# Kernel optimization log

Hardware: AMD Instinct MI355X
Metric: run time of the kernel (lower is better)

## Reference

```python
import jax, jax.numpy as jnp
import numpy as np

N_NODES = 100000
N_EDGES = 3200000
D_IN = 128
D_OUT = 128


def setup_inputs() -> dict:
    key = jax.random.key(0)
    kx, kw, kb, kr, kc, kv = jax.random.split(key, 6)
    x = jax.random.normal(kx, (N_NODES, D_IN), dtype=jnp.float32)
    W = jax.random.normal(kw, (D_OUT, D_IN), dtype=jnp.float32) * (1.0 / np.sqrt(D_IN))
    b = jax.random.normal(kb, (D_OUT,), dtype=jnp.float32) * 0.01
    adj_rows = jax.random.randint(kr, (N_EDGES,), 0, N_NODES, dtype=jnp.int32)
    adj_cols = jax.random.randint(kc, (N_EDGES,), 0, N_NODES, dtype=jnp.int32)
    adj_vals = jax.random.uniform(kv, (N_EDGES,), dtype=jnp.float32)
    return {"x": x, "W": W, "b": b, "adj_rows": adj_rows,
            "adj_cols": adj_cols, "adj_vals": adj_vals}


def reference(x, W, b, adj_rows, adj_cols, adj_vals):
    # linear: out = x @ W.T + b   -> [N, D_OUT]
    out = jnp.einsum('ni,oi->no', x, W) + b
    # spmm(adj, out): row r = sum over edges (r, c, v) of v * out[c]
    gathered = out[adj_cols] * adj_vals[:, None]          # [E, D_OUT]
    agg = jax.ops.segment_sum(gathered, adj_rows, num_segments=x.shape[0])
    return jax.nn.elu(agg)
```

## Files before the change

### kernel.cpp

```cpp
#include <hip/hip_runtime.h>
#include <hip/hip_bf16.h>
#include <cmath>

#define RPB      32
#define FB_CAP   1280
#define SB_SHIFT 11
#define NSB_MAX  64
#define TILE     2048
#define CH_PER_SB 34

typedef __attribute__((ext_vector_type(8))) short short8;
typedef __attribute__((ext_vector_type(4))) float floatx4;

__device__ __forceinline__ unsigned short f2bf(float f) {
    unsigned int u = __float_as_uint(f);
    u += 0x7FFFu + ((u >> 16) & 1u);
    return (unsigned short)(u >> 16);
}

__global__ __launch_bounds__(256) void gemm_mfma_kernel(
    const float* __restrict__ x, const unsigned short* __restrict__ Wbg,
    const float* __restrict__ b, unsigned short* __restrict__ Yb, int N)
{
    __shared__ __align__(16) unsigned short Wb[128][136];
    __shared__ __align__(16) unsigned short Xb[64][136];
    const int t    = threadIdx.x;
    const int wave = t >> 6;
    const int lane = t & 63;
    const int col  = lane & 15;
    const int quad = lane >> 4;
    const int rowbase = blockIdx.x * 64;

#pragma unroll
    for (int i = 0; i < 8; ++i) {
        const int idx = t + 256 * i;
        const int o = idx >> 4, k8 = (idx & 15) * 8;
        *(uint4*)&Wb[o][k8] = *(const uint4*)&Wbg[idx * 8];
    }
#pragma unroll
    for (int i = 0; i < 8; ++i) {
        const int idx = t + 256 * i;
        const int row = idx >> 5, k4 = (idx & 31) * 4;
        const int gr = rowbase + row;
        float4 v = make_float4(0.f, 0.f, 0.f, 0.f);
        if (gr < N) v = *(const float4*)&x[(size_t)gr * 128 + k4];
        Xb[row][k4 + 0] = f2bf(v.x); Xb[row][k4 + 1] = f2bf(v.y);
        Xb[row][k4 + 2] = f2bf(v.z); Xb[row][k4 + 3] = f2bf(v.w);
    }
    __syncthreads();

    float bias[8];
#pragma unroll
    for (int nt = 0; nt < 8; ++nt) bias[nt] = b[nt * 16 + col];

    floatx4 acc[8] = {};
    const int mrow = wave * 16;
#pragma unroll
    for (int k0 = 0; k0 < 128; k0 += 32) {
        const short8 a = *(const short8*)&Xb[mrow + col][k0 + quad * 8];
#pragma unroll
        for (int nt = 0; nt < 8; ++nt) {
            const short8 bf = *(const short8*)&Wb[nt * 16 + col][k0 + quad * 8];
            acc[nt] = __builtin_amdgcn_mfma_f32_16x16x32_bf16(a, bf, acc[nt], 0, 0, 0);
        }
    }
#pragma unroll
    for (int nt = 0; nt < 8; ++nt) {
#pragma unroll
        for (int reg = 0; reg < 4; ++reg)
            Xb[mrow + quad * 4 + reg][nt * 16 + col] = f2bf(acc[nt][reg] + bias[nt]);
    }
    __syncthreads();
#pragma unroll
    for (int i = 0; i < 4; ++i) {
        const int idx = t + 256 * i;
        const int row = idx >> 4, c16 = (idx & 15) * 8;
        const int gr  = rowbase + row;
        if (gr < N)
            *(uint4*)&Yb[(size_t)gr * 128 + c16] = *(const uint4*)&Xb[row][c16];
    }
}

__global__ __launch_bounds__(256) void init_cursor_kernel(
    int* __restrict__ cursor1, int* __restrict__ cursor2, int SB_CAP, int NB,
    const float* __restrict__ W, unsigned short* __restrict__ Wbg)
{
    const int i = blockIdx.x * blockDim.x + threadIdx.x;
    if (i < NSB_MAX) cursor1[i] = i * SB_CAP;
    if (i < NB)      cursor2[i] = i * FB_CAP;
    const int stride = gridDim.x * blockDim.x;
    for (int j = i; j < 128 * 128 / 4; j += stride) {
        const float4 v = ((const float4*)W)[j];
        uint2 u;
        u.x = (unsigned)f2bf(v.x) | ((unsigned)f2bf(v.y) << 16);
        u.y = (unsigned)f2bf(v.z) | ((unsigned)f2bf(v.w) << 16);
        ((uint2*)Wbg)[j] = u;
    }
}

__global__ __launch_bounds__(256) void pass1_kernel(
    const int* __restrict__ rows, const int* __restrict__ cols,
    const float* __restrict__ vals, int* __restrict__ cursor1,
    int2* __restrict__ pairs1, int E)
{
    __shared__ int2 sbuf[TILE];
    __shared__ unsigned char sbin[TILE];
    __shared__ int hist[NSB_MAX], cur[NSB_MAX];
    const int t  = threadIdx.x;
    const int lo = blockIdx.x * TILE;
    const int cnt = min(TILE, E - lo);

    if (t < NSB_MAX) hist[t] = 0;
    __syncthreads();
    for (int i = t; i < cnt; i += 256) {
        const int   r = rows[lo + i];
        const int   c = cols[lo + i];
        const float v = vals[lo + i];
        sbuf[i] = make_int2(((r & 2047) << 17) | c, __float_as_int(v));
        const int bb = r >> SB_SHIFT;
        sbin[i] = (unsigned char)bb;
        atomicAdd(&hist[bb], 1);
    }
    __syncthreads();
    if (t < NSB_MAX) cur[t] = atomicAdd(&cursor1[t], hist[t]);
    __syncthreads();
    for (int i = t; i < cnt; i += 256) {
        const int pos = atomicAdd(&cur[sbin[i]], 1);
        pairs1[pos] = sbuf[i];
    }
}

__global__ __launch_bounds__(256) void pass2_kernel(
    const int* __restrict__ cursor1, int* __restrict__ cursor2,
    const int2* __restrict__ pairs1, int2* __restrict__ pairs2, int SB_CAP)
{
    __shared__ int2 sbuf[TILE];
    __shared__ int hist[64], cur[64];
    const int t   = threadIdx.x;
    const int sb  = blockIdx.x / CH_PER_SB;
    const int ch  = blockIdx.x % CH_PER_SB;
    const int base = sb * SB_CAP;
    const int scnt = cursor1[sb] - base;
    const int csz  = (scnt + CH_PER_SB - 1) / CH_PER_SB;
    const int lo   = ch * csz;
    const int cnt  = max(0, min(csz, scnt - lo));

    if (t < 64) hist[t] = 0;
    __syncthreads();
    for (int i = t; i < cnt; i += 256) {
        const int2 p = pairs1[base + lo + i];
        sbuf[i] = p;
        atomicAdd(&hist[(unsigned)p.x >> 22], 1);
    }
    __syncthreads();
    if (t < 64) cur[t] = atomicAdd(&cursor2[sb * 64 + t], hist[t]);
    __syncthreads();
    for (int i = t; i < cnt; i += 256) {
        const int2 p = sbuf[i];
        const int bb = (unsigned)p.x >> 22;
        const int pos = atomicAdd(&cur[bb], 1);
        pairs2[pos] = make_int2(p.x & 0x3FFFFF, p.y);
    }
}

__global__ __launch_bounds__(256) void sortgather_kernel(
    const int* __restrict__ cursor2, const int2* __restrict__ pairs2,
    const unsigned int* __restrict__ Yu, float* __restrict__ out, int N)
{
    __shared__ __align__(16) int2 sbuf[FB_CAP];
    __shared__ __align__(16) int2 dbuf[FB_CAP + 4];
    __shared__ int hist[RPB];
    __shared__ int off[RPB];
    __shared__ int cur[RPB];
    __shared__ int rowtick;
    const int b    = blockIdx.x;
    const int t    = threadIdx.x;
    const int lane = t & 63;
    const int slot = b * FB_CAP;
    int cnt = cursor2[b] - slot;
    if (cnt > FB_CAP) cnt = FB_CAP;

    if (t < RPB) hist[t] = 0;
    if (t == 0) rowtick = 0;
    __syncthreads();
    for (int i = t; i < cnt; i += 256) {
        const int2 p = pairs2[slot + i];
        sbuf[i] = p;
        atomicAdd(&hist[p.x >> 17], 1);
    }
    __syncthreads();
    if (t == 0) {
        int run = 0;
#pragma unroll
        for (int k = 0; k < RPB; ++k) { off[k] = run; cur[k] = run; run += hist[k]; }
    }
    __syncthreads();
    for (int i = t; i < cnt; i += 256) {
        const int2 p   = sbuf[i];
        const int  pos = atomicAdd(&cur[p.x >> 17], 1);
        dbuf[pos] = make_int2(p.x & 0x1FFFF, p.y);
    }
    if (t < 4) dbuf[cnt + t] = make_int2(0, 0);
    __syncthreads();

    const int sub   = lane >> 4;
    const int qlane = lane & 15;

    for (;;) {
        int rl = 0;
        if (lane == 0) rl = atomicAdd(&rowtick, 1);
        rl = __shfl(rl, 0);
        if (rl >= RPB) break;
        const int gr = b * RPB + rl;
        if (gr >= N) continue;
        const int s = off[rl];
        const int e = s + hist[rl];

        float acc0 = 0.f, acc1 = 0.f, acc2 = 0.f, acc3 = 0.f;
        float acc4 = 0.f, acc5 = 0.f, acc6 = 0.f, acc7 = 0.f;
#pragma unroll 2
        for (int j = s; j < e; j += 4) {
            const int2 p = dbuf[j + sub];
            float v = __int_as_float(p.y);
            v = (j + sub < e) ? v : 0.0f;
            const uint4 y = *(const uint4*)&Yu[((unsigned)p.x << 6) + qlane * 4];
            acc0 = fmaf(v, __uint_as_float(y.x << 16), acc0);
            acc1 = fmaf(v, __uint_as_float(y.x & 0xFFFF0000u), acc1);
            acc2 = fmaf(v, __uint_as_float(y.y << 16), acc2);
            acc3 = fmaf(v, __uint_as_float(y.y & 0xFFFF0000u), acc3);
            acc4 = fmaf(v, __uint_as_float(y.z << 16), acc4);
            acc5 = fmaf(v, __uint_as_float(y.z & 0xFFFF0000u), acc5);
            acc6 = fmaf(v, __uint_as_float(y.w << 16), acc6);
            acc7 = fmaf(v, __uint_as_float(y.w & 0xFFFF0000u), acc7);
        }
        acc0 += __shfl_xor(acc0, 32); acc1 += __shfl_xor(acc1, 32);
        acc2 += __shfl_xor(acc2, 32); acc3 += __shfl_xor(acc3, 32);
        acc4 += __shfl_xor(acc4, 32); acc5 += __shfl_xor(acc5, 32);
        acc6 += __shfl_xor(acc6, 32); acc7 += __shfl_xor(acc7, 32);
        acc0 += __shfl_xor(acc0, 16); acc1 += __shfl_xor(acc1, 16);
        acc2 += __shfl_xor(acc2, 16); acc3 += __shfl_xor(acc3, 16);
        acc4 += __shfl_xor(acc4, 16); acc5 += __shfl_xor(acc5, 16);
        acc6 += __shfl_xor(acc6, 16); acc7 += __shfl_xor(acc7, 16);

        if (lane < 16) {
            float4 o0, o1;
            o0.x = acc0 > 0.f ? acc0 : __expf(acc0) - 1.f;
            o0.y = acc1 > 0.f ? acc1 : __expf(acc1) - 1.f;
            o0.z = acc2 > 0.f ? acc2 : __expf(acc2) - 1.f;
            o0.w = acc3 > 0.f ? acc3 : __expf(acc3) - 1.f;
            o1.x = acc4 > 0.f ? acc4 : __expf(acc4) - 1.f;
            o1.y = acc5 > 0.f ? acc5 : __expf(acc5) - 1.f;
            o1.z = acc6 > 0.f ? acc6 : __expf(acc6) - 1.f;
            o1.w = acc7 > 0.f ? acc7 : __expf(acc7) - 1.f;
            float* po = &out[(size_t)gr * 128 + qlane * 8];
            *(float4*)po       = o0;
            *(float4*)(po + 4) = o1;
        }
    }
}

__global__ __launch_bounds__(256) void gemm_bias_kernel(
    const float* __restrict__ x, const float* __restrict__ W,
    const float* __restrict__ b, float* __restrict__ Y, int N)
{
    __shared__ float Wt[128][130];
    const int tid  = threadIdx.x;
    const int wave = tid >> 6;
    const int lane = tid & 63;
    for (int i = tid; i < 128 * 128; i += 256) {
        const int o = i >> 7, k = i & 127;
        Wt[k][o] = W[i];
    }
    __syncthreads();
    const float2 bv = *(const float2*)&b[2 * lane];
    for (int row = blockIdx.x * 4 + wave; row < N; row += gridDim.x * 4) {
        float acc0 = 0.f, acc1 = 0.f;
        for (int k = 0; k < 128; ++k) {
            const float2 w = *(const float2*)&Wt[k][2 * lane];
            const float xv = x[(size_t)row * 128 + k];
            acc0 = fmaf(xv, w.x, acc0);
            acc1 = fmaf(xv, w.y, acc1);
        }
        float2 o2; o2.x = acc0 + bv.x; o2.y = acc1 + bv.y;
        *(float2*)&Y[(size_t)row * 128 + 2 * lane] = o2;
    }
}

__global__ __launch_bounds__(256) void scatter_kernel(
    const int* __restrict__ rows, const int* __restrict__ cols,
    const float* __restrict__ vals, const float* __restrict__ Y,
    float* __restrict__ out, int E)
{
    const long long gid = (long long)blockIdx.x * blockDim.x + threadIdx.x;
    const int wid  = (int)(gid >> 6);
    const int lane = threadIdx.x & 63;
    if (wid >= E) return;
    const int   r = rows[wid];
    const int   c = cols[wid];
    const float v = vals[wid];
    const float2 y = *(const float2*)&Y[(size_t)c * 128 + 2 * lane];
    float* po = &out[(size_t)r * 128 + 2 * lane];
    atomicAdd(po,     v * y.x);
    atomicAdd(po + 1, v * y.y);
}

__global__ __launch_bounds__(256) void elu_kernel(float* __restrict__ out, int n4)
{
    int i = blockIdx.x * blockDim.x + threadIdx.x;
    const int stride = gridDim.x * blockDim.x;
    float4* p = (float4*)out;
    for (; i < n4; i += stride) {
        float4 v = p[i];
        v.x = v.x > 0.f ? v.x : expf(v.x) - 1.f;
        v.y = v.y > 0.f ? v.y : expf(v.y) - 1.f;
        v.z = v.z > 0.f ? v.z : expf(v.z) - 1.f;
        v.w = v.w > 0.f ? v.w : expf(v.w) - 1.f;
        p[i] = v;
    }
}

extern "C" void kernel_launch(void* const* d_in, const int* in_sizes, int n_in,
                              void* d_out, int out_size, void* d_ws, size_t ws_size,
                              hipStream_t stream)
{
    const float* x    = (const float*)d_in[0];
    const float* W    = (const float*)d_in[1];
    const float* b    = (const float*)d_in[2];
    const int*   rows = (const int*)d_in[3];
    const int*   cols = (const int*)d_in[4];
    const float* vals = (const float*)d_in[5];
    float* out = (float*)d_out;

    const int N   = in_sizes[0] / 128;
    const int E   = in_sizes[3];
    const int NB  = (N + RPB - 1) / RPB;
    const int NSB = (N + (1 << SB_SHIFT) - 1) >> SB_SHIFT;

    const int sb_mean = (E + NSB - 1) / NSB;
    int sbsig = 1; while (sbsig * sbsig < sb_mean) ++sbsig;
    const int SB_CAP = (sb_mean + 10 * sbsig + 63) & ~63;

    auto align256 = [](size_t v) { return (v + 255) & ~(size_t)255; };
    const size_t offPairs2 = 0;
    const size_t szPairs2  = (size_t)NB * FB_CAP * 8;
    const size_t offShared = align256(offPairs2 + szPairs2);
    const size_t szShared  = (size_t)NSB * SB_CAP * 8 > (size_t)N * 256
                           ? (size_t)NSB * SB_CAP * 8 : (size_t)N * 256;
    const size_t offCur1   = align256(offShared + szShared);
    const size_t offCur2   = align256(offCur1 + NSB_MAX * 4);
    const size_t offWb     = align256(offCur2 + (size_t)NB * 4);
    const size_t need      = offWb + 128 * 128 * 2;

    const bool csr_ok = (need <= ws_size) && (NSB <= NSB_MAX) &&
                        ((long long)E <= (long long)NB * 1056) &&
                        (SB_CAP <= CH_PER_SB * TILE);

    if (csr_ok) {
        int2* pairs2        = (int2*)((char*)d_ws + offPairs2);
        int2* pairs1        = (int2*)((char*)d_ws + offShared);
        unsigned short* Yb  = (unsigned short*)((char*)d_ws + offShared);
        int*  cursor1       = (int*)((char*)d_ws + offCur1);
        int*  cursor2       = (int*)((char*)d_ws + offCur2);
        unsigned short* Wbg = (unsigned short*)((char*)d_ws + offWb);

        init_cursor_kernel<<<(NB + 255) / 256, 256, 0, stream>>>(cursor1, cursor2,
                                                                 SB_CAP, NB, W, Wbg);
        pass1_kernel<<<(E + TILE - 1) / TILE, 256, 0, stream>>>(rows, cols, vals,
                                                                cursor1, pairs1, E);
        pass2_kernel<<<NSB * CH_PER_SB, 256, 0, stream>>>(cursor1, cursor2,
                                                          pairs1, pairs2, SB_CAP);
        gemm_mfma_kernel<<<(N + 63) / 64, 256, 0, stream>>>(x, Wbg, b, Yb, N);
        sortgather_kernel<<<NB, 256, 0, stream>>>(cursor2, pairs2,
                                                  (const unsigned int*)Yb, out, N);
    } else {
        float* Y = (float*)d_ws;
        hipMemsetAsync(d_out, 0, (size_t)out_size * sizeof(float), stream);
        gemm_bias_kernel<<<512, 256, 0, stream>>>(x, W, b, Y, N);
        scatter_kernel<<<(E + 3) / 4, 256, 0, stream>>>(rows, cols, vals, Y, out, E);
        elu_kernel<<<1024, 256, 0, stream>>>(out, out_size / 4);
    }
}
```

Before: 314.1 us.

## Locally sort bucket scatter via LDS prefix scan and pad global cursors

In both bucketing passes, each block now computes a wave-level prefix scan of its bin histogram and builds a permutation in shared memory. It then writes edges out in bin-sorted order, so consecutive threads store to contiguous global addresses instead of scattering. The global cursor1 counters are padded to separate cache lines to reduce atomic contention, and the atomic is skipped for empty bins. The cost is an extra LDS pass and barrier per block, plus additional shared memory.

New measurement: 298.7 us. 4.9% less time.

```diff
diff --git a/kernel.cpp b/kernel.cpp
--- a/kernel.cpp
+++ b/kernel.cpp
@@ -8,6 +8,7 @@
 #define NSB_MAX  64
 #define TILE     2048
 #define CH_PER_SB 34
+#define CPAD     32
 
 typedef __attribute__((ext_vector_type(8))) short short8;
 typedef __attribute__((ext_vector_type(4))) float floatx4;
@@ -86,7 +87,7 @@
     const float* __restrict__ W, unsigned short* __restrict__ Wbg)
 {
     const int i = blockIdx.x * blockDim.x + threadIdx.x;
-    if (i < NSB_MAX) cursor1[i] = i * SB_CAP;
+    if (i < NSB_MAX) cursor1[i * CPAD] = i * SB_CAP;
     if (i < NB)      cursor2[i] = i * FB_CAP;
     const int stride = gridDim.x * blockDim.x;
     for (int j = i; j < 128 * 128 / 4; j += stride) {
@@ -105,8 +106,10 @@
 {
     __shared__ int2 sbuf[TILE];
     __shared__ unsigned char sbin[TILE];
-    __shared__ int hist[NSB_MAX], cur[NSB_MAX];
+    __shared__ unsigned short perm[TILE];
+    __shared__ int hist[NSB_MAX], off[NSB_MAX], gbase[NSB_MAX], cur[NSB_MAX];
     const int t  = threadIdx.x;
+    const int lane = t & 63;
     const int lo = blockIdx.x * TILE;
     const int cnt = min(TILE, E - lo);
 
@@ -122,11 +125,28 @@
         atomicAdd(&hist[bb], 1);
     }
     __syncthreads();
-    if (t < NSB_MAX) cur[t] = atomicAdd(&cursor1[t], hist[t]);
+    if (t < NSB_MAX) {
+        const int h = hist[t];
+        int s = h;
+#pragma unroll
+        for (int d = 1; d < NSB_MAX; d <<= 1) {
+            const int n = __shfl_up(s, d);
+            if (lane >= d) s += n;
+        }
+        off[t] = s - h;
+        cur[t] = s - h;
+        if (h > 0) gbase[t] = atomicAdd(&cursor1[t * CPAD], h);
+    }
     __syncthreads();
     for (int i = t; i < cnt; i += 256) {
         const int pos = atomicAdd(&cur[sbin[i]], 1);
-        pairs1[pos] = sbuf[i];
+        perm[pos] = (unsigned short)i;
+    }
+    __syncthreads();
+    for (int i = t; i < cnt; i += 256) {
+        const int src = perm[i];
+        const int bb  = sbin[src];
+        pairs1[gbase[bb] + (i - off[bb])] = sbuf[src];
     }
 }
 
@@ -135,12 +155,14 @@
     const int2* __restrict__ pairs1, int2* __restrict__ pairs2, int SB_CAP)
 {
     __shared__ int2 sbuf[TILE];
-    __shared__ int hist[64], cur[64];
+    __shared__ unsigned short perm[TILE];
+    __shared__ int hist[64], off[64], gbase[64], cur[64];
     const int t   = threadIdx.x;
+    const int lane = t & 63;
     const int sb  = blockIdx.x / CH_PER_SB;
     const int ch  = blockIdx.x % CH_PER_SB;
     const int base = sb * SB_CAP;
-    const int scnt = cursor1[sb] - base;
+    const int scnt = cursor1[sb * CPAD] - base;
     const int csz  = (scnt + CH_PER_SB - 1) / CH_PER_SB;
     const int lo   = ch * csz;
     const int cnt  = max(0, min(csz, scnt - lo));
@@ -153,13 +175,28 @@
         atomicAdd(&hist[(unsigned)p.x >> 22], 1);
     }
     __syncthreads();
-    if (t < 64) cur[t] = atomicAdd(&cursor2[sb * 64 + t], hist[t]);
-    __syncthreads();
-    for (int i = t; i < cnt; i += 256) {
-        const int2 p = sbuf[i];
+    if (t < 64) {
+        const int h = hist[t];
+        int s = h;
+#pragma unroll
+        for (int d = 1; d < 64; d <<= 1) {
+            const int n = __shfl_up(s, d);
+            if (lane >= d) s += n;
+        }
+        off[t] = s - h;
+        cur[t] = s - h;
+        if (h > 0) gbase[t] = atomicAdd(&cursor2[sb * 64 + t], h);
+    }
+    __syncthreads();
+    for (int i = t; i < cnt; i += 256) {
+        const int pos = atomicAdd(&cur[(unsigned)sbuf[i].x >> 22], 1);
+        perm[pos] = (unsigned short)i;
+    }
+    __syncthreads();
+    for (int i = t; i < cnt; i += 256) {
+        const int2 p = sbuf[perm[i]];
         const int bb = (unsigned)p.x >> 22;
-        const int pos = atomicAdd(&cur[bb], 1);
-        pairs2[pos] = make_int2(p.x & 0x3FFFFF, p.y);
+        pairs2[gbase[bb] + (i - off[bb])] = make_int2(p.x & 0x3FFFFF, p.y);
     }
 }
 
@@ -347,7 +384,7 @@
     const size_t szShared  = (size_t)NSB * SB_CAP * 8 > (size_t)N * 256
                            ? (size_t)NSB * SB_CAP * 8 : (size_t)N * 256;
     const size_t offCur1   = align256(offShared + szShared);
-    const size_t offCur2   = align256(offCur1 + NSB_MAX * 4);
+    const size_t offCur2   = align256(offCur1 + (size_t)NSB_MAX * 4 * CPAD);
     const size_t offWb     = align256(offCur2 + (size_t)NB * 4);
     const size_t need      = offWb + 128 * 128 * 2;
 
```
